# Kernel tuning notes

Hardware: AMD Instinct MI355X
Metric: run time of the kernel (lower is better)

The kernel has to match this reference:

```python
import jax, jax.numpy as jnp
import numpy as np

N = 8192
IN_F = 128
OUT_F = 128


def setup_inputs() -> dict:
    key = jax.random.key(0)
    k1, k2, k3, k4 = jax.random.split(key, 4)
    h = jax.random.normal(k1, (N, IN_F), dtype=jnp.float32)
    pos = jax.random.normal(k2, (N, 1, 3), dtype=jnp.float32)
    # xavier_uniform-ish scale for params
    W = jax.random.uniform(k3, (IN_F, OUT_F), dtype=jnp.float32,
                           minval=-1.0, maxval=1.0) * (1.414 * np.sqrt(6.0 / (IN_F + OUT_F)))
    a = jax.random.uniform(k4, (2 * OUT_F + 3, 1), dtype=jnp.float32,
                           minval=-1.0, maxval=1.0) * (1.414 * np.sqrt(6.0 / (2 * OUT_F + 3 + 1)))
    return {"h": h, "pos": pos, "W": W, "a": a}


def reference(h, pos, W, a):
    # Wh: [N, F]
    Wh = h @ W
    F_ = Wh.shape[1]
    a1 = a[:F_, 0]          # weights on Wh[j] (the repeated / neighbor features)
    a2 = a[F_:2 * F_, 0]    # weights on Wh[i] (the repeat_interleaved / center features)
    a3 = a[2 * F_:, 0]      # weights on pos[i] - pos[j]
    p = pos.reshape(-1, 3)  # [N, 3]
    s_j = Wh @ a1           # [N]
    s_i = Wh @ a2           # [N]
    p_a = p @ a3            # [N]
    # e[i, j] = leaky_relu(Wh[j].a1 + Wh[i].a2 + (pos[i]-pos[j]).a3)
    e = jax.nn.leaky_relu(s_i[:, None] + s_j[None, :] + p_a[:, None] - p_a[None, :],
                          negative_slope=0.2)  # [N, N]
    attention = jax.nn.softmax(e, axis=1)
    # eval mode: dropout is identity
    h_prime = attention @ Wh  # [N, F]
    return jax.nn.elu(h_prime)
```

## Files before the change

kernel.cpp:

```cpp
#include <hip/hip_runtime.h>
#include <hip/hip_bf16.h>

#define N 8192
#define F 128
#define JC 16
#define JSLICE (N / JC)

typedef __attribute__((ext_vector_type(4)))  float f32x4;
typedef __attribute__((ext_vector_type(16))) float f32x16;
typedef __attribute__((ext_vector_type(8)))  short short8;

static __device__ __forceinline__ short bf16bits(float x) {
  __hip_bfloat16 b = __float2bfloat16(x);
  return *reinterpret_cast<short*>(&b);
}

__global__ __launch_bounds__(256) void k_gemm_cd(
    const float* __restrict__ h, const float* __restrict__ pos,
    const float* __restrict__ W, const float* __restrict__ a,
    unsigned short* __restrict__ WhTf, float* __restrict__ cArr,
    float* __restrict__ dArr)
{
  __shared__ float Ws[128 * 128];
  const int tid = threadIdx.x;
  const int r0  = blockIdx.x * 16;

  {
    f32x4* Ws4 = (f32x4*)Ws;
    const f32x4* Wg4 = (const f32x4*)W;
#pragma unroll
    for (int q = 0; q < 16; ++q) Ws4[q * 256 + tid] = Wg4[q * 256 + tid];
  }
  __syncthreads();

  const int rg  = tid >> 5;
  const int c32 = tid & 31;

  f32x4 acc0, acc1;
#pragma unroll
  for (int i = 0; i < 4; ++i) { acc0[i] = 0.0f; acc1[i] = 0.0f; }

  const f32x4* h40 = (const f32x4*)(h + (size_t)(r0 + rg * 2) * 128);
  const f32x4* h41 = (const f32x4*)(h + (size_t)(r0 + rg * 2 + 1) * 128);
  const f32x4* Ws4 = (const f32x4*)Ws;

#pragma unroll 4
  for (int k4 = 0; k4 < 32; ++k4) {
    f32x4 hv0 = h40[k4];
    f32x4 hv1 = h41[k4];
#pragma unroll
    for (int e = 0; e < 4; ++e) {
      f32x4 w = Ws4[(k4 * 4 + e) * 32 + c32];
      acc0 += hv0[e] * w;
      acc1 += hv1[e] * w;
    }
  }

  f32x4 a1v = *(const f32x4*)(a + c32 * 4);
  f32x4 a2v = *(const f32x4*)(a + 128 + c32 * 4);
#pragma unroll
  for (int rr = 0; rr < 2; ++rr) {
    f32x4 accR = rr ? acc1 : acc0;
    f32x4 t1 = accR * a1v;
    f32x4 t2 = accR * a2v;
    float s1 = t1[0] + t1[1] + t1[2] + t1[3];
    float s2 = t2[0] + t2[1] + t2[2] + t2[3];
#pragma unroll
    for (int m = 1; m < 32; m <<= 1) {
      s1 += __shfl_xor(s1, m);
      s2 += __shfl_xor(s2, m);
    }
    if (c32 == 0) {
      const int row = r0 + rg * 2 + rr;
      float pa = pos[row * 3 + 0] * a[256] + pos[row * 3 + 1] * a[257] +
                 pos[row * 3 + 2] * a[258];
      cArr[row] = s2 + pa;
      dArr[row] = s1 - pa;
    }
  }

  __syncthreads();
  float* tmp = Ws;
  {
    const int base = (rg * 2) * 132 + c32 * 4;
    *(f32x4*)&tmp[base]       = acc0;
    *(f32x4*)&tmp[base + 132] = acc1;
  }
  __syncthreads();
  {
    const int col  = tid >> 1;
    const int half = tid & 1;
    short8 o;
#pragma unroll
    for (int rr = 0; rr < 8; ++rr)
      o[rr] = bf16bits(tmp[(half * 8 + rr) * 132 + col]);
    *(short8*)(WhTf + (size_t)(r0 >> 4) * 2048 + col * 16 + half * 8) = o;
  }
}

__global__ __launch_bounds__(256, 4) void k_flash(
    const unsigned short* __restrict__ WhTf, const float* __restrict__ cArr,
    const float* __restrict__ dArr, float* __restrict__ pnum,
    float* __restrict__ pden)
{
  __shared__ __align__(16) float dS[JSLICE];

  const int tid = threadIdx.x;
  const int rb  = blockIdx.x & 63;
  const int jc  = blockIdx.x >> 6;
  const int r0  = rb * 128;

  const int w  = tid >> 6;
  const int l  = tid & 63;
  const int cl = l & 31;
  const int kh = l >> 5;

  if (tid < JSLICE / 4)
    ((f32x4*)dS)[tid] = ((const f32x4*)(dArr + (size_t)jc * JSLICE))[tid];
  __syncthreads();

  const float L2E = 1.44269504f;
  const float ci = cArr[r0 + w * 32 + cl] * L2E;

  f32x16 acc0, acc1, acc2, acc3;
#pragma unroll
  for (int i = 0; i < 16; ++i) { acc0[i] = 0; acc1[i] = 0; acc2[i] = 0; acc3[i] = 0; }
  float denA = 0.0f, denB = 0.0f;

  const unsigned short* bPtr =
      WhTf + (size_t)(jc * (JSLICE / 16)) * 2048 + cl * 16 + kh * 8;
  const float* dPtr = dS + kh * 8;

  short8 b0 = *(const short8*)(bPtr);
  short8 b1 = *(const short8*)(bPtr + 512);
  short8 b2 = *(const short8*)(bPtr + 1024);
  short8 b3 = *(const short8*)(bPtr + 1536);
  bPtr += 2048;

  const int iters = JSLICE / 16;
  for (int s = 0; s < iters; ++s) {
    short8 n0 = *(const short8*)(bPtr);
    short8 n1 = *(const short8*)(bPtr + 512);
    short8 n2 = *(const short8*)(bPtr + 1024);
    short8 n3 = *(const short8*)(bPtr + 1536);

    f32x4 dj0 = *(const f32x4*)(dPtr);
    f32x4 dj1 = *(const f32x4*)(dPtr + 4);

    short8 af;
#pragma unroll
    for (int e = 0; e < 8; ++e) {
      float dj = (e < 4) ? dj0[e] : dj1[e - 4];
      float u = __builtin_fmaf(dj, L2E, ci);
      u = fmaxf(u, 0.2f * u);
      float pv = __builtin_amdgcn_exp2f(u);
      if (e & 1) denB += pv; else denA += pv;
      af[e] = bf16bits(pv);
    }

    acc0 = __builtin_amdgcn_mfma_f32_32x32x16_bf16(af, b0, acc0, 0, 0, 0);
    acc1 = __builtin_amdgcn_mfma_f32_32x32x16_bf16(af, b1, acc1, 0, 0, 0);
    acc2 = __builtin_amdgcn_mfma_f32_32x32x16_bf16(af, b2, acc2, 0, 0, 0);
    acc3 = __builtin_amdgcn_mfma_f32_32x32x16_bf16(af, b3, acc3, 0, 0, 0);

    b0 = n0; b1 = n1; b2 = n2; b3 = n3;
    bPtr += 2048; dPtr += 16;
  }

  float den = denA + denB;
  den += __shfl_xor(den, 32);

  {
    float* base = pnum + (size_t)jc * N * F + (size_t)(r0 + w * 32) * 128;
#pragma unroll
    for (int reg = 0; reg < 16; ++reg) {
      const int row = (reg & 3) + 8 * (reg >> 2) + 4 * kh;
      float* rp = base + row * 128 + cl;
      rp[0]  = acc0[reg];
      rp[32] = acc1[reg];
      rp[64] = acc2[reg];
      rp[96] = acc3[reg];
    }
    if (l < 32) pden[(size_t)jc * N + r0 + w * 32 + l] = den;
  }
}

__global__ __launch_bounds__(256) void k_final(
    const float* __restrict__ pnum, const float* __restrict__ pden,
    float* __restrict__ out)
{
  const int g = blockIdx.x * 256 + threadIdx.x;
  const int row = g >> 5;
  f32x4 n;
#pragma unroll
  for (int i = 0; i < 4; ++i) n[i] = 0.0f;
  float dd = 0.0f;
#pragma unroll
  for (int c = 0; c < JC; ++c) {
    n += ((const f32x4*)pnum)[(size_t)c * (N * F / 4) + g];
    dd += pden[(size_t)c * N + row];
  }
  f32x4 r = n * (1.0f / dd);
#pragma unroll
  for (int i = 0; i < 4; ++i) {
    float x = r[i];
    r[i] = x > 0.0f ? x : (__builtin_amdgcn_exp2f(x * 1.44269504f) - 1.0f);
  }
  ((f32x4*)out)[g] = r;
}

extern "C" void kernel_launch(void* const* d_in, const int* in_sizes, int n_in,
                              void* d_out, int out_size, void* d_ws, size_t ws_size,
                              hipStream_t stream)
{
  const float* h   = (const float*)d_in[0];
  const float* pos = (const float*)d_in[1];
  const float* W   = (const float*)d_in[2];
  const float* a   = (const float*)d_in[3];
  float* out = (float*)d_out;

  char* ws = (char*)d_ws;
  unsigned short* WhTf = (unsigned short*)ws;
  float* cArr = (float*)(ws + (size_t)2 * 1024 * 1024);
  float* dArr = cArr + N;
  float* pden = dArr + N;
  float* pnum = pden + (size_t)JC * N;

  hipLaunchKernelGGL(k_gemm_cd, dim3(512), dim3(256), 0, stream,
                     h, pos, W, a, WhTf, cArr, dArr);
  hipLaunchKernelGGL(k_flash, dim3(64 * JC), dim3(256), 0, stream,
                     WhTf, cArr, dArr, pnum, pden);
  hipLaunchKernelGGL(k_final, dim3((N * F / 4) / 256), dim3(256), 0, stream,
                     pnum, pden, out);
}
```

Measured before the change: 111.2 us.

## Store fp16 partial numerators, add row-max shift, larger flash blocks and MFMA priority

```diff
diff --git a/kernel.cpp b/kernel.cpp
--- a/kernel.cpp
+++ b/kernel.cpp
@@ -5,10 +5,12 @@
 #define F 128
 #define JC 16
 #define JSLICE (N / JC)
+#define RB 256
 
 typedef __attribute__((ext_vector_type(4)))  float f32x4;
 typedef __attribute__((ext_vector_type(16))) float f32x16;
 typedef __attribute__((ext_vector_type(8)))  short short8;
+typedef _Float16 f16x8 __attribute__((ext_vector_type(8)));
 
 static __device__ __forceinline__ short bf16bits(float x) {
   __hip_bfloat16 b = __float2bfloat16(x);
@@ -98,17 +100,36 @@
   }
 }
 
-__global__ __launch_bounds__(256, 4) void k_flash(
+__global__ __launch_bounds__(256) void k_dmax(
+    const float* __restrict__ dArr, float* __restrict__ dmaxP)
+{
+  __shared__ float red[4];
+  float m = -1e30f;
+  const f32x4* d4 = (const f32x4*)dArr;
+#pragma unroll
+  for (int q = 0; q < 8; ++q) {
+    f32x4 v = d4[threadIdx.x * 8 + q];
+    m = fmaxf(m, fmaxf(fmaxf(v[0], v[1]), fmaxf(v[2], v[3])));
+  }
+#pragma unroll
+  for (int s = 1; s < 64; s <<= 1) m = fmaxf(m, __shfl_xor(m, s));
+  if ((threadIdx.x & 63) == 0) red[threadIdx.x >> 6] = m;
+  __syncthreads();
+  if (threadIdx.x == 0)
+    dmaxP[0] = fmaxf(fmaxf(red[0], red[1]), fmaxf(red[2], red[3]));
+}
+
+__global__ __launch_bounds__(512, 4) void k_flash(
     const unsigned short* __restrict__ WhTf, const float* __restrict__ cArr,
-    const float* __restrict__ dArr, float* __restrict__ pnum,
-    float* __restrict__ pden)
+    const float* __restrict__ dArr, const float* __restrict__ dmaxP,
+    _Float16* __restrict__ pnum, float* __restrict__ pden)
 {
   __shared__ __align__(16) float dS[JSLICE];
 
   const int tid = threadIdx.x;
-  const int rb  = blockIdx.x & 63;
-  const int jc  = blockIdx.x >> 6;
-  const int r0  = rb * 128;
+  const int rb  = blockIdx.x & 31;
+  const int jc  = blockIdx.x >> 5;
+  const int r0  = rb * RB;
 
   const int w  = tid >> 6;
   const int l  = tid & 63;
@@ -120,7 +141,10 @@
   __syncthreads();
 
   const float L2E = 1.44269504f;
-  const float ci = cArr[r0 + w * 32 + cl] * L2E;
+  const float ci   = cArr[r0 + w * 32 + cl];
+  const float dmax = dmaxP[0];
+  float t0 = ci + dmax;
+  const float negs = -L2E * fmaxf(t0, 0.2f * t0);
 
   f32x16 acc0, acc1, acc2, acc3;
 #pragma unroll
@@ -151,17 +175,19 @@
 #pragma unroll
     for (int e = 0; e < 8; ++e) {
       float dj = (e < 4) ? dj0[e] : dj1[e - 4];
-      float u = __builtin_fmaf(dj, L2E, ci);
-      u = fmaxf(u, 0.2f * u);
-      float pv = __builtin_amdgcn_exp2f(u);
+      float t  = ci + dj;
+      float lr = fmaxf(t, 0.2f * t);
+      float pv = __builtin_amdgcn_exp2f(__builtin_fmaf(lr, L2E, negs));
       if (e & 1) denB += pv; else denA += pv;
       af[e] = bf16bits(pv);
     }
 
+    __builtin_amdgcn_s_setprio(1);
     acc0 = __builtin_amdgcn_mfma_f32_32x32x16_bf16(af, b0, acc0, 0, 0, 0);
     acc1 = __builtin_amdgcn_mfma_f32_32x32x16_bf16(af, b1, acc1, 0, 0, 0);
     acc2 = __builtin_amdgcn_mfma_f32_32x32x16_bf16(af, b2, acc2, 0, 0, 0);
     acc3 = __builtin_amdgcn_mfma_f32_32x32x16_bf16(af, b3, acc3, 0, 0, 0);
+    __builtin_amdgcn_s_setprio(0);
 
     b0 = n0; b1 = n1; b2 = n2; b3 = n3;
     bPtr += 2048; dPtr += 16;
@@ -171,42 +197,50 @@
   den += __shfl_xor(den, 32);
 
   {
-    float* base = pnum + (size_t)jc * N * F + (size_t)(r0 + w * 32) * 128;
+    _Float16* base = pnum + (size_t)jc * N * F + (size_t)(r0 + w * 32) * 128;
 #pragma unroll
     for (int reg = 0; reg < 16; ++reg) {
       const int row = (reg & 3) + 8 * (reg >> 2) + 4 * kh;
-      float* rp = base + row * 128 + cl;
-      rp[0]  = acc0[reg];
-      rp[32] = acc1[reg];
-      rp[64] = acc2[reg];
-      rp[96] = acc3[reg];
+      _Float16* rp = base + row * 128 + cl;
+      rp[0]  = (_Float16)acc0[reg];
+      rp[32] = (_Float16)acc1[reg];
+      rp[64] = (_Float16)acc2[reg];
+      rp[96] = (_Float16)acc3[reg];
     }
     if (l < 32) pden[(size_t)jc * N + r0 + w * 32 + l] = den;
   }
 }
 
 __global__ __launch_bounds__(256) void k_final(
-    const float* __restrict__ pnum, const float* __restrict__ pden,
+    const _Float16* __restrict__ pnum, const float* __restrict__ pden,
     float* __restrict__ out)
 {
-  const int g = blockIdx.x * 256 + threadIdx.x;
-  const int row = g >> 5;
-  f32x4 n;
-#pragma unroll
-  for (int i = 0; i < 4; ++i) n[i] = 0.0f;
+  const int g8 = blockIdx.x * 256 + threadIdx.x;
+  const int row = g8 >> 4;
+  float n[8];
+#pragma unroll
+  for (int i = 0; i < 8; ++i) n[i] = 0.0f;
   float dd = 0.0f;
 #pragma unroll
   for (int c = 0; c < JC; ++c) {
-    n += ((const f32x4*)pnum)[(size_t)c * (N * F / 4) + g];
+    f16x8 hv = ((const f16x8*)(pnum + (size_t)c * N * F))[g8];
+#pragma unroll
+    for (int i = 0; i < 8; ++i) n[i] += (float)hv[i];
     dd += pden[(size_t)c * N + row];
   }
-  f32x4 r = n * (1.0f / dd);
+  const float inv = 1.0f / dd;
+  f32x4 r0, r1;
+#pragma unroll
+  for (int i = 0; i < 4; ++i) { r0[i] = n[i] * inv; r1[i] = n[i + 4] * inv; }
 #pragma unroll
   for (int i = 0; i < 4; ++i) {
-    float x = r[i];
-    r[i] = x > 0.0f ? x : (__builtin_amdgcn_exp2f(x * 1.44269504f) - 1.0f);
-  }
-  ((f32x4*)out)[g] = r;
+    float x = r0[i];
+    r0[i] = x > 0.0f ? x : (__builtin_amdgcn_exp2f(x * 1.44269504f) - 1.0f);
+    float y = r1[i];
+    r1[i] = y > 0.0f ? y : (__builtin_amdgcn_exp2f(y * 1.44269504f) - 1.0f);
+  }
+  ((f32x4*)out)[g8 * 2]     = r0;
+  ((f32x4*)out)[g8 * 2 + 1] = r1;
 }
 
 extern "C" void kernel_launch(void* const* d_in, const int* in_sizes, int n_in,
@@ -223,13 +257,15 @@
   unsigned short* WhTf = (unsigned short*)ws;
   float* cArr = (float*)(ws + (size_t)2 * 1024 * 1024);
   float* dArr = cArr + N;
-  float* pden = dArr + N;
-  float* pnum = pden + (size_t)JC * N;
+  float* dmaxP = dArr + N;
+  float* pden = dmaxP + 4;
+  _Float16* pnum = (_Float16*)(pden + (size_t)JC * N);
 
   hipLaunchKernelGGL(k_gemm_cd, dim3(512), dim3(256), 0, stream,
                      h, pos, W, a, WhTf, cArr, dArr);
-  hipLaunchKernelGGL(k_flash, dim3(64 * JC), dim3(256), 0, stream,
-                     WhTf, cArr, dArr, pnum, pden);
-  hipLaunchKernelGGL(k_final, dim3((N * F / 4) / 256), dim3(256), 0, stream,
+  hipLaunchKernelGGL(k_dmax, dim3(1), dim3(256), 0, stream, dArr, dmaxP);
+  hipLaunchKernelGGL(k_flash, dim3((N / RB) * JC), dim3(512), 0, stream,
+                     WhTf, cArr, dArr, dmaxP, pnum, pden);
+  hipLaunchKernelGGL(k_final, dim3((N * F / 8) / 256), dim3(256), 0, stream,
                      pnum, pden, out);
 }
```

Result: no change. 109.3 us (-1.7%).
